# Kernel optimization log

Measured on AMD Instinct MI355X. Metric: run time of the kernel, lower is better.

The kernel has to match this reference:

```python
import jax, jax.numpy as jnp
import numpy as np

# Dims: lifted grid is N_X x N_Y, input signal has N_IN dims (= N_X*N_Y).
N_X, N_Y, N_IN = 32, 32, 1024
FILT = 33              # resolution-filter taps (odd, centered)
SIGMA0 = 0.1           # resolution_filter_initial_sigma (step 0 of decay schedule)
EPS = 1e-7


def _resolution_filter(sigma):
    # Gaussian taps on normalized coords in ~[-1, 1], normalized to sum 1.
    t = (jnp.arange(FILT, dtype=jnp.float32) - FILT // 2) * (2.0 / FILT)
    k = jnp.exp(-0.5 * jnp.square(t / sigma))
    return k / jnp.sum(k)


def _interpolate_lifting_map(lm_raw, filt):
    # Circular 1-D convolution of the generator parametrization with the
    # Gaussian resolution filter along the input-signal axis.
    P = N_X * N_Y
    pad = FILT // 2
    v = lm_raw.reshape(P, 1, N_IN)
    v = jnp.concatenate([v[..., -pad:], v, v[..., :pad]], axis=-1)  # wrap pad
    k = filt.reshape(1, 1, FILT)
    out = jax.lax.conv_general_dilated(
        v, k, window_strides=(1,), padding='VALID',
        dimension_numbers=('NCH', 'OIH', 'NCH'))
    return out.reshape(N_X, N_Y, N_IN)


def setup_inputs() -> dict:
    key = jax.random.key(0)
    k1, k2 = jax.random.split(key)
    x = jax.random.normal(k1, (16384, N_IN), dtype=jnp.float32)
    lm_raw = jax.random.normal(k2, (N_X, N_Y, N_IN), dtype=jnp.float32) / np.float32(np.sqrt(N_IN))
    return {"x": x, "lm_raw": lm_raw}


def reference(x, lm_raw):
    # _demean_and_normalize_input: per-sample demean + std-normalize.
    mu = jnp.mean(x, axis=-1, keepdims=True)
    sd = jnp.std(x, axis=-1, keepdims=True)
    xn = (x - mu) / (sd + EPS)
    # _sample_resolution_filter + _interpolate_lifting_map
    filt = _resolution_filter(jnp.asarray(SIGMA0, dtype=jnp.float32))
    lm = _interpolate_lifting_map(lm_raw, filt)  # [n_x, n_y, n_in]
    # _lift: y[b, i, j] = sum_n lm[i, j, n] * x[b, n]
    y = jnp.einsum('xyn,bn->bxy', lm, xn)
    return y
```

## Files before the change

kernel.cpp:

```cpp
#include <hip/hip_runtime.h>
#include <hip/hip_bf16.h>

#define N_IN   1024
#define N_P    1024
#define FILT   33
#define PAD    16

typedef __attribute__((ext_vector_type(8))) __bf16 bf16x8;
typedef __attribute__((ext_vector_type(4))) float  f32x4;

#define GLB(p) ((const __attribute__((address_space(1))) unsigned int*)(p))
#define LDSP(p) ((__attribute__((address_space(3))) unsigned int*)(p))

__device__ __forceinline__ unsigned short f2bf(float f) {
    union { __hip_bfloat16 h; unsigned short u; } cv;
    cv.h = __float2bfloat16(f);
    return cv.u;
}

__global__ __launch_bounds__(256)
void normalize_kernel(const float* __restrict__ x, __hip_bfloat16* __restrict__ xn)
{
    const int lane = threadIdx.x & 63;
    const int row  = blockIdx.x * 4 + (threadIdx.x >> 6);

    const float4* xr = reinterpret_cast<const float4*>(x + (size_t)row * N_IN);
    float4 v[4];
    float s = 0.f, s2 = 0.f;
#pragma unroll
    for (int i = 0; i < 4; i++) {
        v[i] = xr[i * 64 + lane];
        s  += v[i].x + v[i].y + v[i].z + v[i].w;
        s2 += v[i].x * v[i].x + v[i].y * v[i].y + v[i].z * v[i].z + v[i].w * v[i].w;
    }
#pragma unroll
    for (int off = 32; off > 0; off >>= 1) {
        s  += __shfl_xor(s,  off, 64);
        s2 += __shfl_xor(s2, off, 64);
    }
    const float mu  = s * (1.0f / N_IN);
    const float var = fmaxf(s2 * (1.0f / N_IN) - mu * mu, 0.0f);
    const float inv = 1.0f / (sqrtf(var) + 1e-7f);

    ushort4* outv = reinterpret_cast<ushort4*>(xn + (size_t)row * N_IN);
#pragma unroll
    for (int i = 0; i < 4; i++) {
        ushort4 o;
        o.x = f2bf((v[i].x - mu) * inv);
        o.y = f2bf((v[i].y - mu) * inv);
        o.z = f2bf((v[i].z - mu) * inv);
        o.w = f2bf((v[i].w - mu) * inv);
        outv[i * 64 + lane] = o;
    }
}

__global__ __launch_bounds__(256)
void conv_kernel(const float* __restrict__ lm_raw, __hip_bfloat16* __restrict__ lm)
{
    __shared__ float row[N_IN];
    __shared__ float fw[FILT];
    const int tid = threadIdx.x;
    const int p   = blockIdx.x;

    if (tid < FILT) {
        float t = (tid - PAD) * (2.0f / FILT);
        float u = t * 10.0f;
        fw[tid] = expf(-0.5f * u * u);
    }
    reinterpret_cast<float4*>(row)[tid] =
        reinterpret_cast<const float4*>(lm_raw + (size_t)p * N_IN)[tid];
    __syncthreads();

    float fsum = 0.f;
#pragma unroll
    for (int f = 0; f < FILT; f++) fsum += fw[f];
    const float inv = 1.0f / fsum;

    const int n0 = tid * 4;
    float o[4] = {0.f, 0.f, 0.f, 0.f};
#pragma unroll
    for (int f = 0; f < FILT; f++) {
        const float w = fw[f];
#pragma unroll
        for (int j = 0; j < 4; j++)
            o[j] += w * row[(n0 + j + f - PAD) & (N_IN - 1)];
    }
    ushort4 ov;
    ov.x = f2bf(o[0] * inv);
    ov.y = f2bf(o[1] * inv);
    ov.z = f2bf(o[2] * inv);
    ov.w = f2bf(o[3] * inv);
    reinterpret_cast<ushort4*>(lm + (size_t)p * N_IN)[tid] = ov;
}

__global__ __launch_bounds__(512, 4)
void gemm_bt3(const __hip_bfloat16* __restrict__ A,
              const __hip_bfloat16* __restrict__ B,
              float* __restrict__ C,
              int M, int N, int K)
{
    constexpr int BK = 32;
    __shared__ char smem[3][24576];

    const int tid = threadIdx.x;
    const int l   = tid & 63;
    const int w   = tid >> 6;
    const int wm  = w >> 1;
    const int wn  = w & 1;

    const int o    = blockIdx.x;
    const int lin  = (o & 7) * (gridDim.x >> 3) + (o >> 3);
    const int tn   = lin & 7;
    const int tm   = lin >> 3;
    const size_t bm = (size_t)tm * 256;
    const size_t bn = (size_t)tn * 128;

    const int srow = w * 16 + (l >> 2);
    const int scol = 16 * ((l & 3) ^ ((l >> 3) & 3));
    const char* gA = (const char*)(A + (bm + srow) * (size_t)K) + scol;
    const char* gB = (const char*)(B + (bn + srow) * (size_t)K) + scol;
    const size_t rowstep = (size_t)128 * K * 2;

#define STAGE(t, b) do {                                                        \
    const char* a0_ = gA + (size_t)(t) * (BK * 2);                              \
    const char* b0_ = gB + (size_t)(t) * (BK * 2);                              \
    char* La_ = &smem[(b)][0]     + w * 1024;                                   \
    char* Lb_ = &smem[(b)][16384] + w * 1024;                                   \
    __builtin_amdgcn_global_load_lds(GLB(a0_),           LDSP(La_),        16, 0, 0); \
    __builtin_amdgcn_global_load_lds(GLB(a0_ + rowstep), LDSP(La_ + 8192), 16, 0, 0); \
    __builtin_amdgcn_global_load_lds(GLB(b0_),           LDSP(Lb_),        16, 0, 0); \
} while (0)

    const int lr = l & 15;
    const int kb = l >> 4;
    const int rslot = 16 * (kb ^ ((lr >> 1) & 3));
    const int abase = (wm * 64 + lr) * 64 + rslot;
    const int bbase = 16384 + (wn * 64 + lr) * 64 + rslot;

    f32x4 acc[4][4] = {};

    const int NT = K / BK;

    STAGE(0, 0);
    STAGE(1, 1);

    int buf = 0;
    for (int t = 0; t < NT; ++t) {
        asm volatile("s_waitcnt lgkmcnt(0)" ::: "memory");
        if (t < NT - 1) asm volatile("s_waitcnt vmcnt(3)" ::: "memory");
        else            asm volatile("s_waitcnt vmcnt(0)" ::: "memory");
        __builtin_amdgcn_s_barrier();
        asm volatile("" ::: "memory");

        {
            const int t2 = t + 2;
            if (t2 < NT) {
                int b2 = buf + 2; if (b2 >= 3) b2 -= 3;
                STAGE(t2, b2);
            }
        }

        const char* Sb = &smem[buf][0];
        bf16x8 afr[4], bfr[4];
#pragma unroll
        for (int n = 0; n < 4; n++) bfr[n] = *(const bf16x8*)(Sb + bbase + n * 1024);
#pragma unroll
        for (int m = 0; m < 4; m++) afr[m] = *(const bf16x8*)(Sb + abase + m * 1024);

        __builtin_amdgcn_s_setprio(1);
#pragma unroll
        for (int m = 0; m < 4; m++)
#pragma unroll
            for (int n = 0; n < 4; n++)
                acc[m][n] = __builtin_amdgcn_mfma_f32_16x16x32_bf16(afr[m], bfr[n], acc[m][n], 0, 0, 0);
        __builtin_amdgcn_s_setprio(0);

        if (++buf == 3) buf = 0;
    }
#undef STAGE

    const int crow = (l >> 4) * 4;
    const int ccol = l & 15;
#pragma unroll
    for (int m = 0; m < 4; m++)
#pragma unroll
        for (int n = 0; n < 4; n++) {
#pragma unroll
            for (int r = 0; r < 4; r++) {
                const size_t row = bm + wm * 64 + m * 16 + crow + r;
                const size_t col = bn + wn * 64 + n * 16 + ccol;
                C[row * N + col] = acc[m][n][r];
            }
        }
}

extern "C" void kernel_launch(void* const* d_in, const int* in_sizes, int n_in,
                              void* d_out, int out_size, void* d_ws, size_t ws_size,
                              hipStream_t stream) {
    const float* x      = (const float*)d_in[0];
    const float* lm_raw = (const float*)d_in[1];
    float* out = (float*)d_out;

    const int M = in_sizes[0] / N_IN;

    __hip_bfloat16* xn = (__hip_bfloat16*)d_ws;
    __hip_bfloat16* lm = (__hip_bfloat16*)((char*)d_ws + (size_t)M * N_IN * 2);

    normalize_kernel<<<M / 4, 256, 0, stream>>>(x, xn);
    conv_kernel<<<N_P, 256, 0, stream>>>(lm_raw, lm);

    const int nblk = (M / 256) * (N_P / 128);
    gemm_bt3<<<nblk, dim3(512), 0, stream>>>(xn, lm, out, M, N_P, N_IN);
}
```

Before: 65.77 us.

## Fuse input normalization into GEMM A-tile loading, keep only per-row stats kernel

Replaces the normalize kernel that wrote a bf16 copy of x with a stats-only kernel producing per-row mean and inverse std. The GEMM now loads fp32 x directly through registers, normalizes and converts to bf16, and writes the A tile into LDS, while B still uses direct global-to-LDS loads. This removes the write and re-read of the normalized intermediate, but doubles the bytes fetched for A inside the GEMM, adds VALU conversion work in the main loop, and lowers the occupancy hint from 4 to 2. It also drops the s_setprio around the MFMA block.

```diff
diff --git a/kernel.cpp b/kernel.cpp
--- a/kernel.cpp
+++ b/kernel.cpp
@@ -12,26 +12,28 @@
 #define GLB(p) ((const __attribute__((address_space(1))) unsigned int*)(p))
 #define LDSP(p) ((__attribute__((address_space(3))) unsigned int*)(p))
 
-__device__ __forceinline__ unsigned short f2bf(float f) {
+__device__ __forceinline__ unsigned int f2bfu(float f) {
     union { __hip_bfloat16 h; unsigned short u; } cv;
     cv.h = __float2bfloat16(f);
-    return cv.u;
+    return (unsigned int)cv.u;
+}
+__device__ __forceinline__ unsigned int pack2bf(float a, float b) {
+    return f2bfu(a) | (f2bfu(b) << 16);
 }
 
 __global__ __launch_bounds__(256)
-void normalize_kernel(const float* __restrict__ x, __hip_bfloat16* __restrict__ xn)
+void stats_kernel(const float* __restrict__ x, float2* __restrict__ muinv)
 {
     const int lane = threadIdx.x & 63;
     const int row  = blockIdx.x * 4 + (threadIdx.x >> 6);
 
     const float4* xr = reinterpret_cast<const float4*>(x + (size_t)row * N_IN);
-    float4 v[4];
     float s = 0.f, s2 = 0.f;
 #pragma unroll
     for (int i = 0; i < 4; i++) {
-        v[i] = xr[i * 64 + lane];
-        s  += v[i].x + v[i].y + v[i].z + v[i].w;
-        s2 += v[i].x * v[i].x + v[i].y * v[i].y + v[i].z * v[i].z + v[i].w * v[i].w;
+        float4 v = xr[i * 64 + lane];
+        s  += v.x + v.y + v.z + v.w;
+        s2 += v.x * v.x + v.y * v.y + v.z * v.z + v.w * v.w;
     }
 #pragma unroll
     for (int off = 32; off > 0; off >>= 1) {
@@ -41,17 +43,7 @@
     const float mu  = s * (1.0f / N_IN);
     const float var = fmaxf(s2 * (1.0f / N_IN) - mu * mu, 0.0f);
     const float inv = 1.0f / (sqrtf(var) + 1e-7f);
-
-    ushort4* outv = reinterpret_cast<ushort4*>(xn + (size_t)row * N_IN);
-#pragma unroll
-    for (int i = 0; i < 4; i++) {
-        ushort4 o;
-        o.x = f2bf((v[i].x - mu) * inv);
-        o.y = f2bf((v[i].y - mu) * inv);
-        o.z = f2bf((v[i].z - mu) * inv);
-        o.w = f2bf((v[i].w - mu) * inv);
-        outv[i * 64 + lane] = o;
-    }
+    if (lane == 0) muinv[row] = make_float2(mu, inv);
 }
 
 __global__ __launch_bounds__(256)
@@ -86,18 +78,19 @@
             o[j] += w * row[(n0 + j + f - PAD) & (N_IN - 1)];
     }
     ushort4 ov;
-    ov.x = f2bf(o[0] * inv);
-    ov.y = f2bf(o[1] * inv);
-    ov.z = f2bf(o[2] * inv);
-    ov.w = f2bf(o[3] * inv);
+    ov.x = (unsigned short)f2bfu(o[0] * inv);
+    ov.y = (unsigned short)f2bfu(o[1] * inv);
+    ov.z = (unsigned short)f2bfu(o[2] * inv);
+    ov.w = (unsigned short)f2bfu(o[3] * inv);
     reinterpret_cast<ushort4*>(lm + (size_t)p * N_IN)[tid] = ov;
 }
 
-__global__ __launch_bounds__(512, 4)
-void gemm_bt3(const __hip_bfloat16* __restrict__ A,
-              const __hip_bfloat16* __restrict__ B,
-              float* __restrict__ C,
-              int M, int N, int K)
+__global__ __launch_bounds__(512, 2)
+void gemm_fused(const float* __restrict__ X,
+                const float2* __restrict__ muinv,
+                const __hip_bfloat16* __restrict__ B,
+                float* __restrict__ C,
+                int M, int N, int K)
 {
     constexpr int BK = 32;
     __shared__ char smem[3][24576];
@@ -115,21 +108,42 @@
     const size_t bm = (size_t)tm * 256;
     const size_t bn = (size_t)tn * 128;
 
-    const int srow = w * 16 + (l >> 2);
-    const int scol = 16 * ((l & 3) ^ ((l >> 3) & 3));
-    const char* gA = (const char*)(A + (bm + srow) * (size_t)K) + scol;
-    const char* gB = (const char*)(B + (bn + srow) * (size_t)K) + scol;
-    const size_t rowstep = (size_t)128 * K * 2;
-
-#define STAGE(t, b) do {                                                        \
-    const char* a0_ = gA + (size_t)(t) * (BK * 2);                              \
-    const char* b0_ = gB + (size_t)(t) * (BK * 2);                              \
-    char* La_ = &smem[(b)][0]     + w * 1024;                                   \
-    char* Lb_ = &smem[(b)][16384] + w * 1024;                                   \
-    __builtin_amdgcn_global_load_lds(GLB(a0_),           LDSP(La_),        16, 0, 0); \
-    __builtin_amdgcn_global_load_lds(GLB(a0_ + rowstep), LDSP(La_ + 8192), 16, 0, 0); \
-    __builtin_amdgcn_global_load_lds(GLB(b0_),           LDSP(Lb_),        16, 0, 0); \
-} while (0)
+    const int arow = tid >> 1;
+    const int kh   = tid & 1;
+    const int akey = (arow >> 1) & 3;
+    const float4* gx = reinterpret_cast<const float4*>(
+        X + (bm + arow) * (size_t)K + kh * 16);
+    const float2 mi  = muinv[bm + arow];
+    const float  amu = mi.x, ainv = mi.y;
+    const int aoff0 = arow * 64 + 16 * ((kh * 2 + 0) ^ akey);
+    const int aoff1 = arow * 64 + 16 * ((kh * 2 + 1) ^ akey);
+
+    float4 a0, a1, a2, a3;
+
+#define LOADA(t) do {                        \
+    const float4* g_ = gx + (size_t)(t) * 8; \
+    a0 = g_[0]; a1 = g_[1]; a2 = g_[2]; a3 = g_[3]; } while (0)
+
+#define WRITEA(b) do {                                                   \
+    uint4 w0_, w1_;                                                      \
+    w0_.x = pack2bf((a0.x - amu) * ainv, (a0.y - amu) * ainv);           \
+    w0_.y = pack2bf((a0.z - amu) * ainv, (a0.w - amu) * ainv);           \
+    w0_.z = pack2bf((a1.x - amu) * ainv, (a1.y - amu) * ainv);           \
+    w0_.w = pack2bf((a1.z - amu) * ainv, (a1.w - amu) * ainv);           \
+    w1_.x = pack2bf((a2.x - amu) * ainv, (a2.y - amu) * ainv);           \
+    w1_.y = pack2bf((a2.z - amu) * ainv, (a2.w - amu) * ainv);           \
+    w1_.z = pack2bf((a3.x - amu) * ainv, (a3.y - amu) * ainv);           \
+    w1_.w = pack2bf((a3.z - amu) * ainv, (a3.w - amu) * ainv);           \
+    *reinterpret_cast<uint4*>(&smem[(b)][aoff0]) = w0_;                  \
+    *reinterpret_cast<uint4*>(&smem[(b)][aoff1]) = w1_; } while (0)
+
+    const int bsrow = w * 16 + (l >> 2);
+    const int bscol = 16 * ((l & 3) ^ ((l >> 3) & 3));
+    const char* gB = (const char*)(B + (bn + bsrow) * (size_t)K) + bscol;
+
+#define STAGEB(t, b) \
+    __builtin_amdgcn_global_load_lds(GLB(gB + (size_t)(t) * (BK * 2)), \
+                                     LDSP(&smem[(b)][16384] + tid * 16), 16, 0, 0)
 
     const int lr = l & 15;
     const int kb = l >> 4;
@@ -138,26 +152,27 @@
     const int bbase = 16384 + (wn * 64 + lr) * 64 + rslot;
 
     f32x4 acc[4][4] = {};
-
     const int NT = K / BK;
 
-    STAGE(0, 0);
-    STAGE(1, 1);
+    LOADA(0);
+    STAGEB(0, 0);
+    WRITEA(0);
+    LOADA(1);
+    STAGEB(1, 1);
 
     int buf = 0;
     for (int t = 0; t < NT; ++t) {
         asm volatile("s_waitcnt lgkmcnt(0)" ::: "memory");
-        if (t < NT - 1) asm volatile("s_waitcnt vmcnt(3)" ::: "memory");
+        if (t < NT - 1) asm volatile("s_waitcnt vmcnt(1)" ::: "memory");
         else            asm volatile("s_waitcnt vmcnt(0)" ::: "memory");
         __builtin_amdgcn_s_barrier();
-        asm volatile("" ::: "memory");
+        __builtin_amdgcn_sched_barrier(0);
 
         {
-            const int t2 = t + 2;
-            if (t2 < NT) {
-                int b2 = buf + 2; if (b2 >= 3) b2 -= 3;
-                STAGE(t2, b2);
-            }
+            int b1 = buf + 1; if (b1 >= 3) b1 -= 3;
+            int b2 = buf + 2; if (b2 >= 3) b2 -= 3;
+            if (t + 1 < NT) WRITEA(b1);
+            if (t + 2 < NT) { LOADA(t + 2); STAGEB(t + 2, b2); }
         }
 
         const char* Sb = &smem[buf][0];
@@ -167,17 +182,17 @@
 #pragma unroll
         for (int m = 0; m < 4; m++) afr[m] = *(const bf16x8*)(Sb + abase + m * 1024);
 
-        __builtin_amdgcn_s_setprio(1);
 #pragma unroll
         for (int m = 0; m < 4; m++)
 #pragma unroll
             for (int n = 0; n < 4; n++)
                 acc[m][n] = __builtin_amdgcn_mfma_f32_16x16x32_bf16(afr[m], bfr[n], acc[m][n], 0, 0, 0);
-        __builtin_amdgcn_s_setprio(0);
 
         if (++buf == 3) buf = 0;
     }
-#undef STAGE
+#undef LOADA
+#undef WRITEA
+#undef STAGEB
 
     const int crow = (l >> 4) * 4;
     const int ccol = l & 15;
@@ -203,12 +218,12 @@
 
     const int M = in_sizes[0] / N_IN;
 
-    __hip_bfloat16* xn = (__hip_bfloat16*)d_ws;
-    __hip_bfloat16* lm = (__hip_bfloat16*)((char*)d_ws + (size_t)M * N_IN * 2);
-
-    normalize_kernel<<<M / 4, 256, 0, stream>>>(x, xn);
+    __hip_bfloat16* lm = (__hip_bfloat16*)d_ws;
+    float2* muinv = (float2*)((char*)d_ws + (size_t)N_P * N_IN * 2);
+
     conv_kernel<<<N_P, 256, 0, stream>>>(lm_raw, lm);
+    stats_kernel<<<M / 4, 256, 0, stream>>>(x, muinv);
 
     const int nblk = (M / 256) * (N_P / 128);
-    gemm_bt3<<<nblk, dim3(512), 0, stream>>>(xn, lm, out, M, N_P, N_IN);
-}
+    gemm_fused<<<nblk, dim3(512), 0, stream>>>(x, muinv, lm, out, M, N_P, N_IN);
+}
```

New measurement: 72.78 us. 1.11x slower.
